# Optimization experiments

Measured on AMD Instinct MI355X. Metric: run time of the kernel, lower is better.

Reference implementation:

```python
import jax, jax.numpy as jnp
import numpy as np

B, N, EMB, H, DH = 1, 196, 256, 8, 32
HID = 4 * EMB
EPS = 1e-5
SCALE = 16.0  # emb_size ** 0.5 (torch code scales by emb_size, not head_dim)


def _ln(x, w, b):
    m = jnp.mean(x, axis=-1, keepdims=True)
    v = jnp.mean((x - m) ** 2, axis=-1, keepdims=True)
    return (x - m) * jax.lax.rsqrt(v + EPS) * w + b


def _qkv(x, W, bias):
    # rearrange 'b n (h d qkv) -> qkv b h n d'
    t = (x @ W + bias).reshape(B, N, H, DH, 3)
    t = jnp.transpose(t, (4, 0, 2, 1, 3))
    return t[0], t[1], t[2]


def _attn(q, k, v, Wp, bp):
    att = jax.nn.softmax(jnp.einsum('bhqd,bhkd->bhqk', q, k) / SCALE, axis=-1)
    o = jnp.einsum('bhqk,bhkd->bhqd', att, v)
    o = jnp.transpose(o, (0, 2, 1, 3)).reshape(B, N, EMB)  # b n (h d)
    return o @ Wp + bp


def _ff(x, W1, b1, W2, b2):
    return jax.nn.gelu(x @ W1 + b1, approximate=False) @ W2 + b2


def _recon(x):
    x = x.reshape(B, 14, 14, 16, 16)
    x = jnp.transpose(x, (0, 3, 4, 1, 2))
    return x.reshape(B, 1, 224, 224)


def setup_inputs() -> dict:
    key = jax.random.key(0)
    ks = jax.random.split(key, 16)
    rn = lambda k, shape: jax.random.normal(k, shape, jnp.float32) * 0.02
    d = {
        'vis_emb': jax.random.normal(ks[0], (B, N, EMB), jnp.float32),
        'ir_emb': jax.random.normal(ks[1], (B, N, EMB), jnp.float32),
        'ln1v_w': jnp.ones((EMB,), jnp.float32), 'ln1v_b': jnp.zeros((EMB,), jnp.float32),
        'ln1i_w': jnp.ones((EMB,), jnp.float32), 'ln1i_b': jnp.zeros((EMB,), jnp.float32),
        'ln2v_w': jnp.ones((EMB,), jnp.float32), 'ln2v_b': jnp.zeros((EMB,), jnp.float32),
        'ln2i_w': jnp.ones((EMB,), jnp.float32), 'ln2i_b': jnp.zeros((EMB,), jnp.float32),
        'Wqkv_v': rn(ks[2], (EMB, 3 * EMB)), 'bqkv_v': jnp.zeros((3 * EMB,), jnp.float32),
        'Wqkv_i': rn(ks[3], (EMB, 3 * EMB)), 'bqkv_i': jnp.zeros((3 * EMB,), jnp.float32),
        'Wp_v': rn(ks[4], (EMB, EMB)), 'bp_v': jnp.zeros((EMB,), jnp.float32),
        'Wp_i': rn(ks[5], (EMB, EMB)), 'bp_i': jnp.zeros((EMB,), jnp.float32),
        'W1v': rn(ks[6], (EMB, HID)), 'b1v': jnp.zeros((HID,), jnp.float32),
        'W2v': rn(ks[7], (HID, EMB)), 'b2v': jnp.zeros((EMB,), jnp.float32),
        'W1i': rn(ks[8], (EMB, HID)), 'b1i': jnp.zeros((HID,), jnp.float32),
        'W2i': rn(ks[9], (HID, EMB)), 'b2i': jnp.zeros((EMB,), jnp.float32),
    }
    return d


def reference(vis_emb, ir_emb, ln1v_w, ln1v_b, ln1i_w, ln1i_b, ln2v_w, ln2v_b,
              ln2i_w, ln2i_b, Wqkv_v, bqkv_v, Wqkv_i, bqkv_i, Wp_v, bp_v,
              Wp_i, bp_i, W1v, b1v, W2v, b2v, W1i, b1i, W2i, b2i):
    nv = _ln(vis_emb, ln1v_w, ln1v_b)
    ni = _ln(ir_emb, ln1i_w, ln1i_b)
    qv, kv_, vv = _qkv(vis_emb, Wqkv_v, bqkv_v)
    qi, ki, vi = _qkv(ir_emb, Wqkv_i, bqkv_i)
    cross_v2i = _attn(qv, ki, vi, Wp_v, bp_v)   # vis queries attend ir k/v
    cross_i2v = _attn(qi, kv_, vv, Wp_i, bp_i)  # ir queries attend vis k/v
    rv = nv + cross_v2i
    ri = ni + cross_i2v
    lv = _ln(rv, ln2v_w, ln2v_b)
    li = _ln(ri, ln2i_w, ln2i_b)
    ov = _ff(lv, W1v, b1v, W2v, b2v) + lv
    oi = _ff(li, W1i, b1i, W2i, b2i) + li
    return jnp.concatenate([_recon(oi), _recon(ov)], axis=1)  # (1,2,224,224)
```

## Files before the change

### kernel.cpp

```cpp
#include <hip/hip_runtime.h>
#include <math.h>

#define NT   196
#define EMB  256
#define NH   8
#define DH   32
#define HID  1024
#define EPSV 1e-5f

#define GEMM_PANEL(Wptr, ldw, xsT, pp, cq, ks, KITER)                          \
    {                                                                          \
        const float* Wb = (Wptr);                                              \
        float4 a0 = {0,0,0,0}, a1 = a0, a2 = a0, a3 = a0;                      \
        _Pragma("unroll 8")                                                    \
        for (int kk = (ks) * (KITER); kk < (ks) * (KITER) + (KITER); kk++) {   \
            float4 w4 = *(const float4*)&Wb[kk * (ldw)];                       \
            float4 xr = *(const float4*)&(xsT)[kk * 4];                        \
            a0.x = fmaf(xr.x, w4.x, a0.x); a0.y = fmaf(xr.x, w4.y, a0.y);      \
            a0.z = fmaf(xr.x, w4.z, a0.z); a0.w = fmaf(xr.x, w4.w, a0.w);      \
            a1.x = fmaf(xr.y, w4.x, a1.x); a1.y = fmaf(xr.y, w4.y, a1.y);      \
            a1.z = fmaf(xr.y, w4.z, a1.z); a1.w = fmaf(xr.y, w4.w, a1.w);      \
            a2.x = fmaf(xr.z, w4.x, a2.x); a2.y = fmaf(xr.z, w4.y, a2.y);      \
            a2.z = fmaf(xr.z, w4.z, a2.z); a2.w = fmaf(xr.z, w4.w, a2.w);      \
            a3.x = fmaf(xr.w, w4.x, a3.x); a3.y = fmaf(xr.w, w4.y, a3.y);      \
            a3.z = fmaf(xr.w, w4.z, a3.z); a3.w = fmaf(xr.w, w4.w, a3.w);      \
        }                                                                      \
        *(float4*)&(pp)[((ks) * 4 + 0) * 256 + (cq) * 4] = a0;                 \
        *(float4*)&(pp)[((ks) * 4 + 1) * 256 + (cq) * 4] = a1;                 \
        *(float4*)&(pp)[((ks) * 4 + 2) * 256 + (cq) * 4] = a2;                 \
        *(float4*)&(pp)[((ks) * 4 + 3) * 256 + (cq) * 4] = a3;                 \
    }

__global__ __launch_bounds__(256) void k1_qkv(
    const float* __restrict__ vis, const float* __restrict__ ir,
    const float* __restrict__ Wqkv_v, const float* __restrict__ bqkv_v,
    const float* __restrict__ Wqkv_i, const float* __restrict__ bqkv_i,
    float* __restrict__ Q, float* __restrict__ Kq, float* __restrict__ Vq)
{
    const int b = blockIdx.x;
    const int s = b / 147;
    const int rem = b % 147;
    const int n0 = (rem / 3) * 4;
    const int cg = rem % 3;
    const int t = threadIdx.x;

    const float* x    = (s == 0) ? vis    : ir;
    const float* W    = (s == 0) ? Wqkv_v : Wqkv_i;
    const float* bias = (s == 0) ? bqkv_v : bqkv_i;

    __shared__ float xsT[EMB * 4];
    __shared__ float pp[4 * 4 * 256];

    {
        int r = t >> 6, c4 = (t & 63) * 4;
        float4 xv = *(const float4*)&x[(n0 + r) * EMB + c4];
        xsT[(c4 + 0) * 4 + r] = xv.x;
        xsT[(c4 + 1) * 4 + r] = xv.y;
        xsT[(c4 + 2) * 4 + r] = xv.z;
        xsT[(c4 + 3) * 4 + r] = xv.w;
    }
    __syncthreads();

    const int cq = t & 63, ks = t >> 6;
    GEMM_PANEL(W + cg * 256 + cq * 4, 768, xsT, pp, cq, ks, 64);
    __syncthreads();

    const int col = cg * 256 + t;
    const int h = col / 96, rr = col % 96, d = rr / 3, q = rr % 3;
    float* dst = (q == 0) ? Q : (q == 1 ? Kq : Vq);
    const float bval = bias[col];
    #pragma unroll
    for (int r = 0; r < 4; r++) {
        float v = pp[(0 * 4 + r) * 256 + t] + pp[(1 * 4 + r) * 256 + t]
                + pp[(2 * 4 + r) * 256 + t] + pp[(3 * 4 + r) * 256 + t] + bval;
        dst[((s * NH + h) * NT + n0 + r) * DH + d] = v;
    }
}

__global__ __launch_bounds__(256) void k2_attn(
    const float* __restrict__ Q, const float* __restrict__ Kq,
    const float* __restrict__ Vq, float* __restrict__ AO)
{
    const int b  = blockIdx.x;
    const int s  = b / 112;
    const int rm = b % 112;
    const int h  = rm / 14;
    const int rt = rm % 14;
    const int t    = threadIdx.x;
    const int wv   = t >> 6;
    const int lane = t & 63;

    __shared__ float kl[NT * 33];
    __shared__ float vl[NT * 33];
    __shared__ float pb[4][NT];

    const float4* Ks4 = (const float4*)(Kq + ((1 - s) * NH + h) * NT * DH);
    const float4* Vs4 = (const float4*)(Vq + ((1 - s) * NH + h) * NT * DH);
    for (int idx = t; idx < NT * 8; idx += 256) {
        int j = idx >> 3, d4 = (idx & 7) * 4;
        float4 kv = Ks4[idx];
        kl[j * 33 + d4 + 0] = kv.x; kl[j * 33 + d4 + 1] = kv.y;
        kl[j * 33 + d4 + 2] = kv.z; kl[j * 33 + d4 + 3] = kv.w;
        float4 vv = Vs4[idx];
        vl[j * 33 + d4 + 0] = vv.x; vl[j * 33 + d4 + 1] = vv.y;
        vl[j * 33 + d4 + 2] = vv.z; vl[j * 33 + d4 + 3] = vv.w;
    }
    __syncthreads();

    const float* Qs = Q + ((s * NH + h) * NT) * DH;
    const bool v3 = (lane + 192) < NT;
    const int  j3 = v3 ? (lane + 192) : 0;

    for (int it = 0; it < 4; it++) {
        int lr = it * 4 + wv;
        bool act = lr < 14;
        int i = rt * 14 + lr;
        float inv_sum = 0.0f;
        if (act) {
            float qreg[DH];
            #pragma unroll
            for (int d = 0; d < DH; d++) qreg[d] = Qs[i * DH + d];
            float s0 = 0.f, s1 = 0.f, s2 = 0.f, s3 = 0.f;
            #pragma unroll
            for (int d = 0; d < DH; d++) {
                float qd = qreg[d];
                s0 = fmaf(qd, kl[(lane      ) * 33 + d], s0);
                s1 = fmaf(qd, kl[(lane +  64) * 33 + d], s1);
                s2 = fmaf(qd, kl[(lane + 128) * 33 + d], s2);
                s3 = fmaf(qd, kl[ j3          * 33 + d], s3);
            }
            const float sc = 1.0f / 16.0f;
            s0 *= sc; s1 *= sc; s2 *= sc; s3 *= sc;
            float m = fmaxf(fmaxf(s0, s1), v3 ? fmaxf(s2, s3) : s2);
            #pragma unroll
            for (int mk = 32; mk >= 1; mk >>= 1) m = fmaxf(m, __shfl_xor(m, mk));
            float p0 = expf(s0 - m), p1 = expf(s1 - m), p2 = expf(s2 - m);
            float p3 = v3 ? expf(s3 - m) : 0.0f;
            float ls = p0 + p1 + p2 + p3;
            #pragma unroll
            for (int mk = 32; mk >= 1; mk >>= 1) ls += __shfl_xor(ls, mk);
            inv_sum = 1.0f / ls;
            pb[wv][lane]       = p0;
            pb[wv][lane +  64] = p1;
            pb[wv][lane + 128] = p2;
            if (v3) pb[wv][lane + 192] = p3;
        }
        __syncthreads();
        if (act) {
            int d = lane & 31, half = lane >> 5;
            float o = 0.0f;
            int jb = half * 98;
            for (int jj = 0; jj < 98; jj++) {
                int j = jb + jj;
                o = fmaf(pb[wv][j], vl[j * 33 + d], o);
            }
            o += __shfl_xor(o, 32);
            if (lane < 32) AO[(s * NT + i) * EMB + h * DH + d] = o * inv_sum;
        }
        __syncthreads();
    }
}

__global__ __launch_bounds__(256) void k3_projln(
    const float* __restrict__ vis, const float* __restrict__ ir,
    const float* __restrict__ AO,
    const float* __restrict__ ln1v_w, const float* __restrict__ ln1v_b,
    const float* __restrict__ ln1i_w, const float* __restrict__ ln1i_b,
    const float* __restrict__ Wp_v, const float* __restrict__ bp_v,
    const float* __restrict__ Wp_i, const float* __restrict__ bp_i,
    const float* __restrict__ ln2v_w, const float* __restrict__ ln2v_b,
    const float* __restrict__ ln2i_w, const float* __restrict__ ln2i_b,
    float* __restrict__ LV)
{
    const int b = blockIdx.x;
    const int s = b / 49;
    const int n0 = (b % 49) * 4;
    const int t = threadIdx.x;

    const float* x   = (s == 0) ? vis    : ir;
    const float* Wp  = (s == 0) ? Wp_v   : Wp_i;
    const float* bp  = (s == 0) ? bp_v   : bp_i;
    const float* l1w = (s == 0) ? ln1v_w : ln1i_w;
    const float* l1b = (s == 0) ? ln1v_b : ln1i_b;
    const float* l2w = (s == 0) ? ln2v_w : ln2i_w;
    const float* l2b = (s == 0) ? ln2v_b : ln2i_b;

    __shared__ float aoT[EMB * 4];
    __shared__ float nvb[4 * 256];
    __shared__ float rbuf[4 * 256];
    __shared__ float pp[4 * 4 * 256];

    const int r = t >> 6, lane = t & 63, c4 = lane * 4;
    const int cq = t & 63, ks = t >> 6;

    {
        float4 xv = *(const float4*)&x[(n0 + r) * EMB + c4];
        float sum = xv.x + xv.y + xv.z + xv.w;
        float sq  = xv.x*xv.x + xv.y*xv.y + xv.z*xv.z + xv.w*xv.w;
        #pragma unroll
        for (int mk = 32; mk >= 1; mk >>= 1) {
            sum += __shfl_xor(sum, mk);
            sq  += __shfl_xor(sq,  mk);
        }
        float mean = sum * (1.0f / EMB);
        float inv  = rsqrtf(sq * (1.0f / EMB) - mean * mean + EPSV);
        float4 wv4 = *(const float4*)&l1w[c4];
        float4 bv4 = *(const float4*)&l1b[c4];
        nvb[r * 256 + c4 + 0] = (xv.x - mean) * inv * wv4.x + bv4.x;
        nvb[r * 256 + c4 + 1] = (xv.y - mean) * inv * wv4.y + bv4.y;
        nvb[r * 256 + c4 + 2] = (xv.z - mean) * inv * wv4.z + bv4.z;
        nvb[r * 256 + c4 + 3] = (xv.w - mean) * inv * wv4.w + bv4.w;
        float4 av = *(const float4*)&AO[(s * NT + n0 + r) * EMB + c4];
        aoT[(c4 + 0) * 4 + r] = av.x;
        aoT[(c4 + 1) * 4 + r] = av.y;
        aoT[(c4 + 2) * 4 + r] = av.z;
        aoT[(c4 + 3) * 4 + r] = av.w;
    }
    __syncthreads();

    GEMM_PANEL(Wp + cq * 4, EMB, aoT, pp, cq, ks, 64);
    __syncthreads();

    {
        const float bval = bp[t];
        #pragma unroll
        for (int r2 = 0; r2 < 4; r2++) {
            float v = pp[(0 * 4 + r2) * 256 + t] + pp[(1 * 4 + r2) * 256 + t]
                    + pp[(2 * 4 + r2) * 256 + t] + pp[(3 * 4 + r2) * 256 + t]
                    + bval + nvb[r2 * 256 + t];
            rbuf[r2 * 256 + t] = v;
        }
    }
    __syncthreads();
    {
        float4 rv = *(const float4*)&rbuf[r * 256 + c4];
        float sum = rv.x + rv.y + rv.z + rv.w;
        float sq  = rv.x*rv.x + rv.y*rv.y + rv.z*rv.z + rv.w*rv.w;
        #pragma unroll
        for (int mk = 32; mk >= 1; mk >>= 1) {
            sum += __shfl_xor(sum, mk);
            sq  += __shfl_xor(sq,  mk);
        }
        float mean = sum * (1.0f / EMB);
        float inv  = rsqrtf(sq * (1.0f / EMB) - mean * mean + EPSV);
        float4 wv4 = *(const float4*)&l2w[c4];
        float4 bv4 = *(const float4*)&l2b[c4];
        float4 o;
        o.x = (rv.x - mean) * inv * wv4.x + bv4.x;
        o.y = (rv.y - mean) * inv * wv4.y + bv4.y;
        o.z = (rv.z - mean) * inv * wv4.z + bv4.z;
        o.w = (rv.w - mean) * inv * wv4.w + bv4.w;
        *(float4*)&LV[(s * NT + n0 + r) * EMB + c4] = o;
    }
}

__global__ __launch_bounds__(256) void k4_ffn(
    const float* __restrict__ LV,
    const float* __restrict__ W1v, const float* __restrict__ b1v,
    const float* __restrict__ W1i, const float* __restrict__ b1i,
    const float* __restrict__ W2v, const float* __restrict__ W2i,
    float* __restrict__ P)
{
    const int b = blockIdx.x;
    const int s = b / 196;
    const int rem = b % 196;
    const int n0 = (rem / 4) * 4;
    const int strip = rem % 4;
    const int col0 = strip * 256;
    const int t = threadIdx.x;

    const float* W1  = (s == 0) ? W1v : W1i;
    const float* bb1 = (s == 0) ? b1v : b1i;
    const float* W2  = (s == 0) ? W2v : W2i;

    __shared__ float lvT[EMB * 4];
    __shared__ float hhT[256 * 4];
    __shared__ float pp[4 * 4 * 256];

    {
        int r = t >> 6, c4 = (t & 63) * 4;
        float4 xv = *(const float4*)&LV[(s * NT + n0 + r) * EMB + c4];
        lvT[(c4 + 0) * 4 + r] = xv.x;
        lvT[(c4 + 1) * 4 + r] = xv.y;
        lvT[(c4 + 2) * 4 + r] = xv.z;
        lvT[(c4 + 3) * 4 + r] = xv.w;
    }
    __syncthreads();

    const int cq = t & 63, ks = t >> 6;

    GEMM_PANEL(W1 + col0 + cq * 4, HID, lvT, pp, cq, ks, 64);
    __syncthreads();

    {
        const float bval = bb1[col0 + t];
        const float kg = 0.7071067811865475f;
        float4 h;
        #pragma unroll
        for (int r = 0; r < 4; r++) {
            float v = pp[(0 * 4 + r) * 256 + t] + pp[(1 * 4 + r) * 256 + t]
                    + pp[(2 * 4 + r) * 256 + t] + pp[(3 * 4 + r) * 256 + t] + bval;
            ((float*)&h)[r] = 0.5f * v * (1.0f + erff(v * kg));
        }
        *(float4*)&hhT[t * 4] = h;
    }
    __syncthreads();

    GEMM_PANEL(W2 + col0 * EMB + cq * 4, EMB, hhT, pp, cq, ks, 64);
    __syncthreads();

    {
        float* Pd = P + (size_t)strip * (2 * NT * EMB);
        #pragma unroll
        for (int r = 0; r < 4; r++) {
            float v = pp[(0 * 4 + r) * 256 + t] + pp[(1 * 4 + r) * 256 + t]
                    + pp[(2 * 4 + r) * 256 + t] + pp[(3 * 4 + r) * 256 + t];
            Pd[(s * NT + n0 + r) * EMB + t] = v;
        }
    }
}

__global__ __launch_bounds__(256) void k5_reduce(
    const float* __restrict__ P, const float* __restrict__ LV,
    const float* __restrict__ b2v, const float* __restrict__ b2i,
    float* __restrict__ out)
{
    const int b = blockIdx.x;
    const int s = b / 49;
    const int n0 = (b % 49) * 4;
    const int t = threadIdx.x;
    const float* bb2 = (s == 0) ? b2v : b2i;

    const float bval = bb2[t];
    const int p1 = t >> 4, p2 = t & 15;
    const int ch = (s == 0) ? 1 : 0;
    const size_t SP = (size_t)2 * NT * EMB;
    #pragma unroll
    for (int r = 0; r < 4; r++) {
        int n = n0 + r;
        size_t base = (size_t)(s * NT + n) * EMB + t;
        float v = P[base] + P[SP + base] + P[2 * SP + base] + P[3 * SP + base]
                + LV[base] + bval;
        int n1 = n / 14, n2 = n % 14;
        int f = p1 * 3136 + p2 * 196 + n1 * 14 + n2;
        out[ch * 50176 + f] = v;
    }
}

extern "C" void kernel_launch(void* const* d_in, const int* in_sizes, int n_in,
                              void* d_out, int out_size, void* d_ws, size_t ws_size,
                              hipStream_t stream)
{
    const float* vis    = (const float*)d_in[0];
    const float* ir     = (const float*)d_in[1];
    const float* ln1v_w = (const float*)d_in[2];
    const float* ln1v_b = (const float*)d_in[3];
    const float* ln1i_w = (const float*)d_in[4];
    const float* ln1i_b = (const float*)d_in[5];
    const float* ln2v_w = (const float*)d_in[6];
    const float* ln2v_b = (const float*)d_in[7];
    const float* ln2i_w = (const float*)d_in[8];
    const float* ln2i_b = (const float*)d_in[9];
    const float* Wqkv_v = (const float*)d_in[10];
    const float* bqkv_v = (const float*)d_in[11];
    const float* Wqkv_i = (const float*)d_in[12];
    const float* bqkv_i = (const float*)d_in[13];
    const float* Wp_v   = (const float*)d_in[14];
    const float* bp_v   = (const float*)d_in[15];
    const float* Wp_i   = (const float*)d_in[16];
    const float* bp_i   = (const float*)d_in[17];
    const float* W1v    = (const float*)d_in[18];
    const float* b1v    = (const float*)d_in[19];
    const float* W2v    = (const float*)d_in[20];
    const float* b2v    = (const float*)d_in[21];
    const float* W1i    = (const float*)d_in[22];
    const float* b1i    = (const float*)d_in[23];
    const float* W2i    = (const float*)d_in[24];
    const float* b2i    = (const float*)d_in[25];

    float* ws = (float*)d_ws;
    float* Q  = ws;
    float* K  = ws + 100352;
    float* V  = ws + 200704;
    float* AO = ws + 301056;
    float* LV = ws + 401408;
    float* P  = ws + 501760;

    k1_qkv<<<294, 256, 0, stream>>>(vis, ir, Wqkv_v, bqkv_v, Wqkv_i, bqkv_i, Q, K, V);
    k2_attn<<<224, 256, 0, stream>>>(Q, K, V, AO);
    k3_projln<<<98, 256, 0, stream>>>(vis, ir, AO,
                                      ln1v_w, ln1v_b, ln1i_w, ln1i_b,
                                      Wp_v, bp_v, Wp_i, bp_i,
                                      ln2v_w, ln2v_b, ln2i_w, ln2i_b, LV);
    k4_ffn<<<392, 256, 0, stream>>>(LV, W1v, b1v, W1i, b1i, W2v, W2i, P);
    k5_reduce<<<98, 256, 0, stream>>>(P, LV, b2v, b2i, (float*)d_out);
}
```

Measured before the change: 161.1 us.

## Fuse projection+LayerNorm kernel into FFN kernel, recomputing per strip

Merges the attention-projection/LayerNorm kernel into the FFN kernel. Each of the 392 blocks recomputes the Wp projection and both LayerNorms for its 4 tokens, then feeds the result straight into the W1/W2 panels from shared memory. Only strip 0 writes LV for the final reduce. This drops one kernel launch and the LV round trip, at the cost of doing the projection GEMM four times redundantly. The GEMM inner loop unroll is also raised from 8 to 16.

```diff
diff --git a/kernel.cpp b/kernel.cpp
--- a/kernel.cpp
+++ b/kernel.cpp
@@ -12,7 +12,7 @@
     {                                                                          \
         const float* Wb = (Wptr);                                              \
         float4 a0 = {0,0,0,0}, a1 = a0, a2 = a0, a3 = a0;                      \
-        _Pragma("unroll 8")                                                    \
+        _Pragma("unroll 16")                                                   \
         for (int kk = (ks) * (KITER); kk < (ks) * (KITER) + (KITER); kk++) {   \
             float4 w4 = *(const float4*)&Wb[kk * (ldw)];                       \
             float4 xr = *(const float4*)&(xsT)[kk * 4];                        \
@@ -161,7 +161,7 @@
     }
 }
 
-__global__ __launch_bounds__(256) void k3_projln(
+__global__ __launch_bounds__(256) void k4_ffn(
     const float* __restrict__ vis, const float* __restrict__ ir,
     const float* __restrict__ AO,
     const float* __restrict__ ln1v_w, const float* __restrict__ ln1v_b,
@@ -170,11 +170,17 @@
     const float* __restrict__ Wp_i, const float* __restrict__ bp_i,
     const float* __restrict__ ln2v_w, const float* __restrict__ ln2v_b,
     const float* __restrict__ ln2i_w, const float* __restrict__ ln2i_b,
-    float* __restrict__ LV)
+    const float* __restrict__ W1v, const float* __restrict__ b1v,
+    const float* __restrict__ W1i, const float* __restrict__ b1i,
+    const float* __restrict__ W2v, const float* __restrict__ W2i,
+    float* __restrict__ LV, float* __restrict__ P)
 {
     const int b = blockIdx.x;
-    const int s = b / 49;
-    const int n0 = (b % 49) * 4;
+    const int s = b / 196;
+    const int rem = b % 196;
+    const int n0 = (rem / 4) * 4;
+    const int strip = rem % 4;
+    const int col0 = strip * 256;
     const int t = threadIdx.x;
 
     const float* x   = (s == 0) ? vis    : ir;
@@ -184,6 +190,9 @@
     const float* l1b = (s == 0) ? ln1v_b : ln1i_b;
     const float* l2w = (s == 0) ? ln2v_w : ln2i_w;
     const float* l2b = (s == 0) ? ln2v_b : ln2i_b;
+    const float* W1  = (s == 0) ? W1v    : W1i;
+    const float* bb1 = (s == 0) ? b1v    : b1i;
+    const float* W2  = (s == 0) ? W2v    : W2i;
 
     __shared__ float aoT[EMB * 4];
     __shared__ float nvb[4 * 256];
@@ -220,7 +229,6 @@
 
     GEMM_PANEL(Wp + cq * 4, EMB, aoT, pp, cq, ks, 64);
     __syncthreads();
-
     {
         const float bval = bp[t];
         #pragma unroll
@@ -232,6 +240,7 @@
         }
     }
     __syncthreads();
+
     {
         float4 rv = *(const float4*)&rbuf[r * 256 + c4];
         float sum = rv.x + rv.y + rv.z + rv.w;
@@ -250,72 +259,42 @@
         o.y = (rv.y - mean) * inv * wv4.y + bv4.y;
         o.z = (rv.z - mean) * inv * wv4.z + bv4.z;
         o.w = (rv.w - mean) * inv * wv4.w + bv4.w;
-        *(float4*)&LV[(s * NT + n0 + r) * EMB + c4] = o;
-    }
-}
-
-__global__ __launch_bounds__(256) void k4_ffn(
-    const float* __restrict__ LV,
-    const float* __restrict__ W1v, const float* __restrict__ b1v,
-    const float* __restrict__ W1i, const float* __restrict__ b1i,
-    const float* __restrict__ W2v, const float* __restrict__ W2i,
-    float* __restrict__ P)
-{
-    const int b = blockIdx.x;
-    const int s = b / 196;
-    const int rem = b % 196;
-    const int n0 = (rem / 4) * 4;
-    const int strip = rem % 4;
-    const int col0 = strip * 256;
-    const int t = threadIdx.x;
-
-    const float* W1  = (s == 0) ? W1v : W1i;
-    const float* bb1 = (s == 0) ? b1v : b1i;
-    const float* W2  = (s == 0) ? W2v : W2i;
-
-    __shared__ float lvT[EMB * 4];
-    __shared__ float hhT[256 * 4];
-    __shared__ float pp[4 * 4 * 256];
-
-    {
-        int r = t >> 6, c4 = (t & 63) * 4;
-        float4 xv = *(const float4*)&LV[(s * NT + n0 + r) * EMB + c4];
-        lvT[(c4 + 0) * 4 + r] = xv.x;
-        lvT[(c4 + 1) * 4 + r] = xv.y;
-        lvT[(c4 + 2) * 4 + r] = xv.z;
-        lvT[(c4 + 3) * 4 + r] = xv.w;
-    }
-    __syncthreads();
-
-    const int cq = t & 63, ks = t >> 6;
-
-    GEMM_PANEL(W1 + col0 + cq * 4, HID, lvT, pp, cq, ks, 64);
-    __syncthreads();
-
+        __syncthreads();
+        aoT[(c4 + 0) * 4 + r] = o.x;
+        aoT[(c4 + 1) * 4 + r] = o.y;
+        aoT[(c4 + 2) * 4 + r] = o.z;
+        aoT[(c4 + 3) * 4 + r] = o.w;
+        if (strip == 0)
+            *(float4*)&LV[(s * NT + n0 + r) * EMB + c4] = o;
+    }
+    __syncthreads();
+
+    GEMM_PANEL(W1 + col0 + cq * 4, HID, aoT, pp, cq, ks, 64);
+    __syncthreads();
     {
         const float bval = bb1[col0 + t];
         const float kg = 0.7071067811865475f;
         float4 h;
         #pragma unroll
-        for (int r = 0; r < 4; r++) {
-            float v = pp[(0 * 4 + r) * 256 + t] + pp[(1 * 4 + r) * 256 + t]
-                    + pp[(2 * 4 + r) * 256 + t] + pp[(3 * 4 + r) * 256 + t] + bval;
-            ((float*)&h)[r] = 0.5f * v * (1.0f + erff(v * kg));
-        }
-        *(float4*)&hhT[t * 4] = h;
-    }
-    __syncthreads();
-
-    GEMM_PANEL(W2 + col0 * EMB + cq * 4, EMB, hhT, pp, cq, ks, 64);
-    __syncthreads();
-
+        for (int r2 = 0; r2 < 4; r2++) {
+            float v = pp[(0 * 4 + r2) * 256 + t] + pp[(1 * 4 + r2) * 256 + t]
+                    + pp[(2 * 4 + r2) * 256 + t] + pp[(3 * 4 + r2) * 256 + t] + bval;
+            ((float*)&h)[r2] = 0.5f * v * (1.0f + erff(v * kg));
+        }
+        __syncthreads();
+        *(float4*)&rbuf[t * 4] = h;
+    }
+    __syncthreads();
+
+    GEMM_PANEL(W2 + col0 * EMB + cq * 4, EMB, rbuf, pp, cq, ks, 64);
+    __syncthreads();
     {
         float* Pd = P + (size_t)strip * (2 * NT * EMB);
         #pragma unroll
-        for (int r = 0; r < 4; r++) {
-            float v = pp[(0 * 4 + r) * 256 + t] + pp[(1 * 4 + r) * 256 + t]
-                    + pp[(2 * 4 + r) * 256 + t] + pp[(3 * 4 + r) * 256 + t];
-            Pd[(s * NT + n0 + r) * EMB + t] = v;
+        for (int r2 = 0; r2 < 4; r2++) {
+            float v = pp[(0 * 4 + r2) * 256 + t] + pp[(1 * 4 + r2) * 256 + t]
+                    + pp[(2 * 4 + r2) * 256 + t] + pp[(3 * 4 + r2) * 256 + t];
+            Pd[(s * NT + n0 + r2) * EMB + t] = v;
         }
     }
 }
@@ -388,10 +367,10 @@
 
     k1_qkv<<<294, 256, 0, stream>>>(vis, ir, Wqkv_v, bqkv_v, Wqkv_i, bqkv_i, Q, K, V);
     k2_attn<<<224, 256, 0, stream>>>(Q, K, V, AO);
-    k3_projln<<<98, 256, 0, stream>>>(vis, ir, AO,
-                                      ln1v_w, ln1v_b, ln1i_w, ln1i_b,
-                                      Wp_v, bp_v, Wp_i, bp_i,
-                                      ln2v_w, ln2v_b, ln2i_w, ln2i_b, LV);
-    k4_ffn<<<392, 256, 0, stream>>>(LV, W1v, b1v, W1i, b1i, W2v, W2i, P);
+    k4_ffn<<<392, 256, 0, stream>>>(vis, ir, AO,
+                                    ln1v_w, ln1v_b, ln1i_w, ln1i_b,
+                                    Wp_v, bp_v, Wp_i, bp_i,
+                                    ln2v_w, ln2v_b, ln2i_w, ln2i_b,
+                                    W1v, b1v, W1i, b1i, W2v, W2i, LV, P);
     k5_reduce<<<98, 256, 0, stream>>>(P, LV, b2v, b2i, (float*)d_out);
 }
```

Result: slower. 167.7 us (+4.1%).
